# Optimization experiments

Hardware: AMD Instinct MI355X
Metric: run time of the kernel (lower is better)

Reference implementation:

```python
import jax, jax.numpy as jnp
import numpy as np

EPS = 1e-8  # torch F.cosine_similarity eps


def setup_inputs() -> dict:
    key = jax.random.key(0)
    ks = jax.random.split(key, 5)
    S, Q, D_in, D, N_WAY, K_SHOT = 100, 4096, 21168, 64, 20, 5
    return {
        "support_images": jax.random.normal(ks[0], (S, D_in), dtype=jnp.float32),
        "support_labels": jax.random.randint(ks[1], (S,), 0, N_WAY),
        "query_images": jax.random.normal(ks[2], (Q, D_in), dtype=jnp.float32),
        "n_way": N_WAY,
        "k_shot": K_SHOT,
        "backbone_w": jax.random.normal(ks[3], (D_in, D), dtype=jnp.float32) * 0.02,
        "backbone_b": jax.random.normal(ks[4], (D,), dtype=jnp.float32) * 0.02,
    }


def _l2_normalize(x):
    # matches torch cosine_similarity: x / max(||x||, eps)
    n = jnp.maximum(jnp.linalg.norm(x, axis=-1, keepdims=True), EPS)
    return x / n


def reference(support_images, support_labels, query_images, n_way, k_shot,
              backbone_w, backbone_b):
    # Backbone: linear embedding (stand-in for conv feature extractor)
    support_emb = support_images @ backbone_w + backbone_b   # [S, D]
    query_emb = query_images @ backbone_w + backbone_b       # [Q, D]

    # Cosine similarity between every query and every support sample: [Q, S]
    sims = _l2_normalize(query_emb) @ _l2_normalize(support_emb).T

    # Softmax over the support axis (per query), as in the original loop
    attn = jax.nn.softmax(sims, axis=1)                      # [Q, S]

    # Per-label scatter-add == one-hot segment-sum: [Q, n_way]
    one_hot = jax.nn.one_hot(support_labels, n_way, dtype=attn.dtype)  # [S, n_way]
    logits = attn @ one_hot
    return logits
```

## Files before the change

kernel.cpp:

```cpp
#include <hip/hip_runtime.h>
#include <hip/hip_bf16.h>
#include <math.h>

#define DEMB 64
#define BM   64
#define KSMAX 32
#define APAD 40

using short8 = __attribute__((ext_vector_type(8))) short;
using u16x8  = __attribute__((ext_vector_type(8))) unsigned short;
using f32x4  = __attribute__((ext_vector_type(4))) float;

__device__ __forceinline__ u16x8 cvt_bf8(float4 a0, float4 a1) {
    union { u16x8 s; __hip_bfloat16 h[8]; } u;
    u.h[0] = __float2bfloat16(a0.x);
    u.h[1] = __float2bfloat16(a0.y);
    u.h[2] = __float2bfloat16(a0.z);
    u.h[3] = __float2bfloat16(a0.w);
    u.h[4] = __float2bfloat16(a1.x);
    u.h[5] = __float2bfloat16(a1.y);
    u.h[6] = __float2bfloat16(a1.z);
    u.h[7] = __float2bfloat16(a1.w);
    return u.s;
}

__global__ __launch_bounds__(256) void prep_wt(
    const float* __restrict__ W, unsigned short* __restrict__ Wt,
    int Din, int Wstride)
{
    __shared__ unsigned short tile[64][65];
    const int k0 = blockIdx.x * 64;
    const int tid = threadIdx.x;
    #pragma unroll
    for (int i = 0; i < 16; ++i) {
        int kk = i * 4 + (tid >> 6);
        int c  = tid & 63;
        int k  = k0 + kk;
        float x = (k < Din) ? W[(size_t)k * DEMB + c] : 0.f;
        union { unsigned short u; __hip_bfloat16 h; } cv;
        cv.h = __float2bfloat16(x);
        tile[kk][c] = cv.u;
    }
    __syncthreads();
    #pragma unroll
    for (int i = 0; i < 16; ++i) {
        int c  = i * 4 + (tid >> 6);
        int kk = tid & 63;
        Wt[(size_t)c * Wstride + k0 + kk] = tile[kk][c];
    }
}

__global__ __launch_bounds__(256) void gemm_mfma(
    const float* __restrict__ Xq, const float* __restrict__ Xs,
    const unsigned short* __restrict__ Wt,
    float* __restrict__ qpart, float* __restrict__ spart,
    int Q, int S, int Din, int Wstride, int nQb, int cpk, int nchunk)
{
    __shared__ unsigned short As[2][BM * APAD];
    __shared__ unsigned short Ws[2][64 * APAD];

    const int tid  = threadIdx.x;
    const int wave = tid >> 6;
    const int lane = tid & 63;
    const int kg   = blockIdx.y;

    const bool isS = (int)blockIdx.x >= nQb;
    const float* X = isS ? Xs : Xq;
    const int nrows = isS ? S : Q;
    const int r0 = (isS ? ((int)blockIdx.x - nQb) : (int)blockIdx.x) * BM;
    float* part = isS ? spart : qpart;
    const int prow = isS ? 128 : Q;

    const int srow = tid >> 2;
    const int sk   = (tid & 3) * 8;
    const bool aval = (r0 + srow) < nrows;
    const float* aptr = X + (size_t)(r0 + srow) * Din;
    const unsigned short* wptr = Wt + (size_t)srow * Wstride + sk;

    const int col16 = lane & 15;
    const int frow  = 16 * wave + col16;
    const int fk    = (lane >> 4) * 8;

    f32x4 acc[4] = { {0.f,0.f,0.f,0.f}, {0.f,0.f,0.f,0.f},
                     {0.f,0.f,0.f,0.f}, {0.f,0.f,0.f,0.f} };

    const int c0 = kg * cpk;
    int c1 = c0 + cpk; if (c1 > nchunk) c1 = nchunk;

    {
        const int k0 = c0 * 32;
        const int kk = k0 + sk;
        float4 a0 = {}, a1 = {};
        if (aval && kk + 8 <= Din) {
            a0 = *reinterpret_cast<const float4*>(aptr + kk);
            a1 = *reinterpret_cast<const float4*>(aptr + kk + 4);
        }
        u16x8 wv = *reinterpret_cast<const u16x8*>(wptr + k0);
        *reinterpret_cast<u16x8*>(&As[0][srow * APAD + sk]) = cvt_bf8(a0, a1);
        *reinterpret_cast<u16x8*>(&Ws[0][srow * APAD + sk]) = wv;
        __syncthreads();
    }

    int cur = 0;
    for (int c = c0; c < c1; ++c) {
        const int cn = c + 1;
        const bool pf = (cn < c1);
        float4 a0 = {}, a1 = {};
        u16x8 wv = {0,0,0,0,0,0,0,0};
        if (pf) {
            const int k0 = cn * 32;
            const int kk = k0 + sk;
            if (aval && kk + 8 <= Din) {
                a0 = *reinterpret_cast<const float4*>(aptr + kk);
                a1 = *reinterpret_cast<const float4*>(aptr + kk + 4);
            }
            wv = *reinterpret_cast<const u16x8*>(wptr + k0);
        }

        short8 af = *reinterpret_cast<const short8*>(&As[cur][frow * APAD + fk]);
        #pragma unroll
        for (int cb = 0; cb < 4; ++cb) {
            short8 bf = *reinterpret_cast<const short8*>(
                &Ws[cur][(16 * cb + col16) * APAD + fk]);
            acc[cb] = __builtin_amdgcn_mfma_f32_16x16x32_bf16(af, bf, acc[cb], 0, 0, 0);
        }

        if (pf) {
            *reinterpret_cast<u16x8*>(&As[cur ^ 1][srow * APAD + sk]) = cvt_bf8(a0, a1);
            *reinterpret_cast<u16x8*>(&Ws[cur ^ 1][srow * APAD + sk]) = wv;
        }
        __syncthreads();
        cur ^= 1;
    }

    #pragma unroll
    for (int cb = 0; cb < 4; ++cb) {
        #pragma unroll
        for (int i = 0; i < 4; ++i) {
            int row = r0 + 16 * wave + (lane >> 4) * 4 + i;
            if (row < nrows)
                part[((size_t)kg * prow + row) * DEMB + 16 * cb + col16] = acc[cb][i];
        }
    }
}

__global__ void support_finalize(const float* __restrict__ spart,
                                 const float* __restrict__ bias,
                                 float* __restrict__ sn, int S, int nkg)
{
    int s = blockIdx.x;
    int c = threadIdx.x;
    float e = bias[c];
    for (int g = 0; g < nkg; ++g)
        e += spart[((size_t)g * 128 + s) * DEMB + c];
    float ss = e * e;
    #pragma unroll
    for (int o = 32; o >= 1; o >>= 1) ss += __shfl_xor(ss, o, 64);
    sn[(size_t)s * DEMB + c] = e / fmaxf(sqrtf(ss), 1e-8f);
}

__global__ __launch_bounds__(256) void attend(
    const float* __restrict__ qpart, const float* __restrict__ sn_g,
    const float* __restrict__ bias, const int* __restrict__ labels,
    const int* __restrict__ p_nway, float* __restrict__ out,
    int S, int Q, int nkg)
{
    __shared__ float sn[100][65];
    __shared__ float qn[4][64];
    __shared__ float bins[4][32];
    __shared__ int   lab[100];

    const int tid  = threadIdx.x;
    const int w    = tid >> 6;
    const int lane = tid & 63;
    const int nw   = *p_nway;

    for (int i = tid; i < S * DEMB; i += 256) sn[i >> 6][i & 63] = sn_g[i];
    if (tid < S) lab[tid] = labels[tid];

    const int q = blockIdx.x * 4 + w;

    float e = bias[lane];
    for (int g = 0; g < nkg; ++g)
        e += qpart[((size_t)g * Q + q) * DEMB + lane];
    float ss = e * e;
    #pragma unroll
    for (int o = 32; o >= 1; o >>= 1) ss += __shfl_xor(ss, o, 64);
    e /= fmaxf(sqrtf(ss), 1e-8f);
    qn[w][lane] = e;
    if (lane < 32) bins[w][lane] = 0.f;
    __syncthreads();

    const bool v1 = (lane + 64) < S;
    const int  s1 = v1 ? lane + 64 : 0;
    float sim0 = 0.f, sim1 = 0.f;
    #pragma unroll 8
    for (int c = 0; c < DEMB; ++c) {
        float qc = qn[w][c];
        sim0 += qc * sn[lane][c];
        sim1 += qc * sn[s1][c];
    }
    if (!v1) sim1 = -INFINITY;

    float lm = fmaxf(sim0, sim1);
    #pragma unroll
    for (int o = 32; o >= 1; o >>= 1) lm = fmaxf(lm, __shfl_xor(lm, o, 64));
    float e0 = __expf(sim0 - lm);
    float e1 = v1 ? __expf(sim1 - lm) : 0.f;
    float d = e0 + e1;
    #pragma unroll
    for (int o = 32; o >= 1; o >>= 1) d += __shfl_xor(d, o, 64);

    atomicAdd(&bins[w][lab[lane]], e0);
    if (v1) atomicAdd(&bins[w][lab[s1]], e1);
    __syncthreads();

    if (lane < nw) out[(size_t)q * nw + lane] = bins[w][lane] / d;
}

extern "C" void kernel_launch(void* const* d_in, const int* in_sizes, int n_in,
                              void* d_out, int out_size, void* d_ws, size_t ws_size,
                              hipStream_t stream)
{
    const float* sup    = (const float*)d_in[0];
    const int*   labels = (const int*)d_in[1];
    const float* qry    = (const float*)d_in[2];
    const int*   p_nway = (const int*)d_in[3];
    const float* W      = (const float*)d_in[5];
    const float* bias   = (const float*)d_in[6];
    float* out = (float*)d_out;

    const int D   = DEMB;
    const int Din = in_sizes[5] / D;
    const int Q   = in_sizes[2] / Din;
    const int S   = in_sizes[1];

    const int nchunk  = (Din + 31) / 32;
    const int Wstride = nchunk * 32;

    char* wsb = (char*)d_ws;
    size_t wt_bytes = (size_t)64 * Wstride * sizeof(unsigned short);
    wt_bytes = (wt_bytes + 255) & ~(size_t)255;
    size_t sn_bytes = (size_t)S * D * sizeof(float);
    sn_bytes = (sn_bytes + 255) & ~(size_t)255;
    size_t per_ks = ((size_t)Q * D + 128 * D) * sizeof(float);

    size_t fixed = wt_bytes + sn_bytes;
    int ks = 1;
    if (ws_size > fixed + per_ks) {
        size_t avail = (ws_size - fixed) / per_ks;
        ks = (int)(avail < KSMAX ? avail : KSMAX);
        if (ks < 1) ks = 1;
    }
    const int cpk = (nchunk + ks - 1) / ks;
    const int nkg = (nchunk + cpk - 1) / cpk;

    unsigned short* Wt = (unsigned short*)wsb;
    float* sn    = (float*)(wsb + wt_bytes);
    float* spart = (float*)(wsb + wt_bytes + sn_bytes);
    float* qpart = spart + (size_t)nkg * 128 * D;

    hipLaunchKernelGGL(prep_wt, dim3((Din + 63) / 64), dim3(256), 0, stream,
                       W, Wt, Din, Wstride);

    const int nQb = (Q + BM - 1) / BM;
    const int nSb = (S + BM - 1) / BM;
    hipLaunchKernelGGL(gemm_mfma, dim3(nQb + nSb, nkg), dim3(256), 0, stream,
                       qry, sup, Wt, qpart, spart, Q, S, Din, Wstride, nQb, cpk, nchunk);

    hipLaunchKernelGGL(support_finalize, dim3(S), dim3(64), 0, stream,
                       spart, bias, sn, S, nkg);

    hipLaunchKernelGGL(attend, dim3(Q / 4), dim3(256), 0, stream,
                       qpart, sn, bias, labels, p_nway, out, S, Q, nkg);
}
```

Measured before the change: 134.5 us.

## Stage GEMM tiles with direct global-to-LDS loads and pre-packed bf16 weights

```diff
diff --git a/kernel.cpp b/kernel.cpp
--- a/kernel.cpp
+++ b/kernel.cpp
@@ -4,8 +4,8 @@
 
 #define DEMB 64
 #define BM   64
+#define BKF  64
 #define KSMAX 32
-#define APAD 40
 
 using short8 = __attribute__((ext_vector_type(8))) short;
 using u16x8  = __attribute__((ext_vector_type(8))) unsigned short;
@@ -24,40 +24,36 @@
     return u.s;
 }
 
+__device__ __forceinline__ void gl16(const void* gsrc, void* lds) {
+    __builtin_amdgcn_global_load_lds(
+        (const __attribute__((address_space(1))) unsigned int*)gsrc,
+        (__attribute__((address_space(3))) unsigned int*)lds,
+        16, 0, 0);
+}
+
 __global__ __launch_bounds__(256) void prep_wt(
-    const float* __restrict__ W, unsigned short* __restrict__ Wt,
-    int Din, int Wstride)
-{
-    __shared__ unsigned short tile[64][65];
-    const int k0 = blockIdx.x * 64;
-    const int tid = threadIdx.x;
-    #pragma unroll
-    for (int i = 0; i < 16; ++i) {
-        int kk = i * 4 + (tid >> 6);
-        int c  = tid & 63;
-        int k  = k0 + kk;
+    const float* __restrict__ W, unsigned short* __restrict__ Wtk, int Din)
+{
+    const int t = blockIdx.x * 256 + threadIdx.x;
+    const int oct = t >> 6, c = t & 63;
+    union { u16x8 v; __hip_bfloat16 h[8]; } u;
+    #pragma unroll
+    for (int j = 0; j < 8; ++j) {
+        int k = oct * 8 + j;
         float x = (k < Din) ? W[(size_t)k * DEMB + c] : 0.f;
-        union { unsigned short u; __hip_bfloat16 h; } cv;
-        cv.h = __float2bfloat16(x);
-        tile[kk][c] = cv.u;
-    }
-    __syncthreads();
-    #pragma unroll
-    for (int i = 0; i < 16; ++i) {
-        int c  = i * 4 + (tid >> 6);
-        int kk = tid & 63;
-        Wt[(size_t)c * Wstride + k0 + kk] = tile[kk][c];
-    }
+        u.h[j] = __float2bfloat16(x);
+    }
+    *reinterpret_cast<u16x8*>(&Wtk[(size_t)t * 8]) = u.v;
 }
 
 __global__ __launch_bounds__(256) void gemm_mfma(
     const float* __restrict__ Xq, const float* __restrict__ Xs,
-    const unsigned short* __restrict__ Wt,
+    const unsigned short* __restrict__ Wtk,
     float* __restrict__ qpart, float* __restrict__ spart,
-    int Q, int S, int Din, int Wstride, int nQb, int cpk, int nchunk)
-{
-    __shared__ unsigned short As[2][BM * APAD];
-    __shared__ unsigned short Ws[2][64 * APAD];
+    int Q, int S, int Din, int nQb, int cpk, int nbatch)
+{
+    __shared__ float          As[2][BM * BKF];
+    __shared__ unsigned short Bs[2][8 * 64 * 8];
 
     const int tid  = threadIdx.x;
     const int wave = tid >> 6;
@@ -71,11 +67,8 @@
     float* part = isS ? spart : qpart;
     const int prow = isS ? 128 : Q;
 
-    const int srow = tid >> 2;
-    const int sk   = (tid & 3) * 8;
-    const bool aval = (r0 + srow) < nrows;
-    const float* aptr = X + (size_t)(r0 + srow) * Din;
-    const unsigned short* wptr = Wt + (size_t)srow * Wstride + sk;
+    const int g  = lane >> 4;
+    const int qp = lane & 15;
 
     const int col16 = lane & 15;
     const int frow  = 16 * wave + col16;
@@ -84,54 +77,60 @@
     f32x4 acc[4] = { {0.f,0.f,0.f,0.f}, {0.f,0.f,0.f,0.f},
                      {0.f,0.f,0.f,0.f}, {0.f,0.f,0.f,0.f} };
 
-    const int c0 = kg * cpk;
-    int c1 = c0 + cpk; if (c1 > nchunk) c1 = nchunk;
-
-    {
-        const int k0 = c0 * 32;
-        const int kk = k0 + sk;
-        float4 a0 = {}, a1 = {};
-        if (aval && kk + 8 <= Din) {
-            a0 = *reinterpret_cast<const float4*>(aptr + kk);
-            a1 = *reinterpret_cast<const float4*>(aptr + kk + 4);
-        }
-        u16x8 wv = *reinterpret_cast<const u16x8*>(wptr + k0);
-        *reinterpret_cast<u16x8*>(&As[0][srow * APAD + sk]) = cvt_bf8(a0, a1);
-        *reinterpret_cast<u16x8*>(&Ws[0][srow * APAD + sk]) = wv;
-        __syncthreads();
-    }
+    const int b0 = kg * cpk;
+    int b1 = b0 + cpk; if (b1 > nbatch) b1 = nbatch;
+
+#define STAGE(P, B) do {                                                       \
+    const int kb_ = (B) * BKF;                                                 \
+    _Pragma("unroll")                                                          \
+    for (int i = 0; i < 4; ++i) {                                              \
+        int rg_ = r0 + 16 * wave + 4 * i + g;                                  \
+        if (rg_ >= nrows) rg_ = nrows - 1;                                     \
+        const int q_ = qp ^ (4 * i + g);                                       \
+        int kq_ = kb_ + 4 * q_;                                                \
+        if (kq_ >= Din) kq_ = 0;                                               \
+        gl16(X + (size_t)rg_ * Din + kq_,                                      \
+             &As[P][(16 * wave + 4 * i) * BKF]);                               \
+    }                                                                          \
+    _Pragma("unroll")                                                          \
+    for (int j = 0; j < 2; ++j) {                                              \
+        gl16(Wtk + ((size_t)((B) * 8 + 2 * wave + j) * 64 + lane) * 8,         \
+             &Bs[P][(2 * wave + j) * 512]);                                    \
+    }                                                                          \
+} while (0)
+
+#define COMPUTE(P, CC) do {                                                    \
+    const int qa_ = (CC) * 8 + (fk >> 2);                                      \
+    const float* Ab_ = &As[P][frow * BKF];                                     \
+    float4 fa_ = *reinterpret_cast<const float4*>(Ab_ + ((qa_    ) ^ col16) * 4); \
+    float4 fb_ = *reinterpret_cast<const float4*>(Ab_ + ((qa_ + 1) ^ col16) * 4); \
+    u16x8 afu_ = cvt_bf8(fa_, fb_);                                            \
+    short8 af_ = (short8)afu_;                                                 \
+    const int ob_ = ((CC) * 4 + (fk >> 3)) * 64;                               \
+    short8 b0_ = *reinterpret_cast<const short8*>(&Bs[P][(ob_ +  0 + col16) * 8]); \
+    short8 b1_ = *reinterpret_cast<const short8*>(&Bs[P][(ob_ + 16 + col16) * 8]); \
+    short8 b2_ = *reinterpret_cast<const short8*>(&Bs[P][(ob_ + 32 + col16) * 8]); \
+    short8 b3_ = *reinterpret_cast<const short8*>(&Bs[P][(ob_ + 48 + col16) * 8]); \
+    acc[0] = __builtin_amdgcn_mfma_f32_16x16x32_bf16(af_, b0_, acc[0], 0, 0, 0);  \
+    acc[1] = __builtin_amdgcn_mfma_f32_16x16x32_bf16(af_, b1_, acc[1], 0, 0, 0);  \
+    acc[2] = __builtin_amdgcn_mfma_f32_16x16x32_bf16(af_, b2_, acc[2], 0, 0, 0);  \
+    acc[3] = __builtin_amdgcn_mfma_f32_16x16x32_bf16(af_, b3_, acc[3], 0, 0, 0);  \
+} while (0)
+
+    STAGE(0, b0);
+    __syncthreads();
 
     int cur = 0;
-    for (int c = c0; c < c1; ++c) {
-        const int cn = c + 1;
-        const bool pf = (cn < c1);
-        float4 a0 = {}, a1 = {};
-        u16x8 wv = {0,0,0,0,0,0,0,0};
-        if (pf) {
-            const int k0 = cn * 32;
-            const int kk = k0 + sk;
-            if (aval && kk + 8 <= Din) {
-                a0 = *reinterpret_cast<const float4*>(aptr + kk);
-                a1 = *reinterpret_cast<const float4*>(aptr + kk + 4);
-            }
-            wv = *reinterpret_cast<const u16x8*>(wptr + k0);
-        }
-
-        short8 af = *reinterpret_cast<const short8*>(&As[cur][frow * APAD + fk]);
-        #pragma unroll
-        for (int cb = 0; cb < 4; ++cb) {
-            short8 bf = *reinterpret_cast<const short8*>(
-                &Ws[cur][(16 * cb + col16) * APAD + fk]);
-            acc[cb] = __builtin_amdgcn_mfma_f32_16x16x32_bf16(af, bf, acc[cb], 0, 0, 0);
-        }
-
-        if (pf) {
-            *reinterpret_cast<u16x8*>(&As[cur ^ 1][srow * APAD + sk]) = cvt_bf8(a0, a1);
-            *reinterpret_cast<u16x8*>(&Ws[cur ^ 1][srow * APAD + sk]) = wv;
-        }
+    for (int b = b0; b < b1; ++b) {
+        if (b + 1 < b1) STAGE(cur ^ 1, b + 1);
+        COMPUTE(cur, 0);
+        COMPUTE(cur, 1);
         __syncthreads();
         cur ^= 1;
     }
+
+#undef STAGE
+#undef COMPUTE
 
     #pragma unroll
     for (int cb = 0; cb < 4; ++cb) {
@@ -235,11 +234,11 @@
     const int Q   = in_sizes[2] / Din;
     const int S   = in_sizes[1];
 
-    const int nchunk  = (Din + 31) / 32;
-    const int Wstride = nchunk * 32;
+    const int nbatch = (Din + BKF - 1) / BKF;
+    const int Koct   = nbatch * 8;
 
     char* wsb = (char*)d_ws;
-    size_t wt_bytes = (size_t)64 * Wstride * sizeof(unsigned short);
+    size_t wt_bytes = (size_t)Koct * 64 * 16;
     wt_bytes = (wt_bytes + 255) & ~(size_t)255;
     size_t sn_bytes = (size_t)S * D * sizeof(float);
     sn_bytes = (sn_bytes + 255) & ~(size_t)255;
@@ -252,21 +251,21 @@
         ks = (int)(avail < KSMAX ? avail : KSMAX);
         if (ks < 1) ks = 1;
     }
-    const int cpk = (nchunk + ks - 1) / ks;
-    const int nkg = (nchunk + cpk - 1) / cpk;
-
-    unsigned short* Wt = (unsigned short*)wsb;
+    const int cpk = (nbatch + ks - 1) / ks;
+    const int nkg = (nbatch + cpk - 1) / cpk;
+
+    unsigned short* Wtk = (unsigned short*)wsb;
     float* sn    = (float*)(wsb + wt_bytes);
     float* spart = (float*)(wsb + wt_bytes + sn_bytes);
     float* qpart = spart + (size_t)nkg * 128 * D;
 
-    hipLaunchKernelGGL(prep_wt, dim3((Din + 63) / 64), dim3(256), 0, stream,
-                       W, Wt, Din, Wstride);
+    hipLaunchKernelGGL(prep_wt, dim3((Koct * 64) / 256), dim3(256), 0, stream,
+                       W, Wtk, Din);
 
     const int nQb = (Q + BM - 1) / BM;
     const int nSb = (S + BM - 1) / BM;
     hipLaunchKernelGGL(gemm_mfma, dim3(nQb + nSb, nkg), dim3(256), 0, stream,
-                       qry, sup, Wt, qpart, spart, Q, S, Din, Wstride, nQb, cpk, nchunk);
+                       qry, sup, Wtk, qpart, spart, Q, S, Din, nQb, cpk, nbatch);
 
     hipLaunchKernelGGL(support_finalize, dim3(S), dim3(64), 0, stream,
                        spart, bias, sn, S, nkg);
```

New measurement: 119.8 us. 1.12x faster.
